# Kernel optimization log

Hardware: AMD Instinct MI355X
Metric: run time of the kernel (lower is better)

Reference implementation:

```python
import jax, jax.numpy as jnp
import numpy as np

N_NODES = 10000
N_EDGES = 640000
D = 128
N_GRAPHS = 16
N_CLASSES = 10


def setup_inputs() -> dict:
    key = jax.random.key(0)
    ks = jax.random.split(key, 12)
    x = jax.random.normal(ks[0], (N_NODES, D), dtype=jnp.float32)
    edge_index = jax.random.randint(ks[1], (2, N_EDGES), 0, N_NODES, dtype=jnp.int64)
    batch_ids = jnp.sort(jax.random.randint(ks[2], (N_NODES,), 0, N_GRAPHS, dtype=jnp.int64))
    s = 1.0 / np.sqrt(D)
    W_in = jax.random.normal(ks[3], (D, D), dtype=jnp.float32) * s
    W_self = jax.random.normal(ks[4], (D, D), dtype=jnp.float32) * s
    b = jnp.zeros((D,), dtype=jnp.float32)
    W_e1 = jax.random.normal(ks[5], (2 * D, D), dtype=jnp.float32) * (1.0 / np.sqrt(2 * D))
    b_e1 = jnp.zeros((D,), dtype=jnp.float32)
    W_e2 = jax.random.normal(ks[6], (D, 1), dtype=jnp.float32) * s
    b_e2 = jnp.zeros((1,), dtype=jnp.float32)
    W_cls = jax.random.normal(ks[7], (D, N_CLASSES), dtype=jnp.float32) * s
    b_cls = jnp.zeros((N_CLASSES,), dtype=jnp.float32)
    return {"x": x, "edge_index": edge_index, "batch_ids": batch_ids,
            "W_in": W_in, "W_self": W_self, "b": b,
            "W_e1": W_e1, "b_e1": b_e1, "W_e2": W_e2, "b_e2": b_e2,
            "W_cls": W_cls, "b_cls": b_cls}


def reference(x, edge_index, batch_ids, W_in, W_self, b, W_e1, b_e1, W_e2, b_e2, W_cls, b_cls):
    src, dst = edge_index[0], edge_index[1]
    # --- gnn(data) -> (z_node, z_graph) : GCN-style message passing ---
    h = x @ W_in                                  # [N, D]
    agg = jax.ops.segment_sum(h[src], dst, num_segments=N_NODES)  # [N, D]
    z_node = jax.nn.relu(agg + x @ W_self + b)    # [N, D]
    # mean pool per graph -> z_graph [B, D]
    sums = jax.ops.segment_sum(z_node, batch_ids, num_segments=N_GRAPHS)
    counts = jax.ops.segment_sum(jnp.ones((N_NODES,), dtype=z_node.dtype), batch_ids, num_segments=N_GRAPHS)
    z_graph = sums / jnp.maximum(counts, 1.0)[:, None]
    # --- edge predictor: gather, concat, MLP ---
    edge_features = jnp.concatenate([z_node[src], z_node[dst]], axis=1)  # [E, 2D]
    pred_edge = jax.nn.relu(edge_features @ W_e1 + b_e1) @ W_e2 + b_e2   # [E, 1]
    # --- classifier ---
    pred_class = z_graph @ W_cls + b_cls          # [B, n_classes]
    return (pred_edge, pred_class)
```

## Files before the change

kernel.cpp:

```cpp
#include <hip/hip_runtime.h>

#define N_NODES   10000
#define N_EDGES   640000
#define DIM       128
#define N_GRAPHS  16
#define N_CLASSES 10

typedef unsigned int uint;
typedef unsigned short ushort;

__device__ __forceinline__ float bf2f(uint lo16) {
    return __uint_as_float(lo16 << 16);
}
__device__ __forceinline__ ushort f2bf(float f) {
    uint u = __float_as_uint(f);
    u += 0x7fffu + ((u >> 16) & 1u);
    return (ushort)(u >> 16);
}

__global__ __launch_bounds__(256) void hist_dst(
    const int* __restrict__ dst, int* __restrict__ cnt)
{
    const int base = (blockIdx.x * 256 + threadIdx.x) * 4;
    const int d0 = dst[base + 0];
    const int d1 = dst[base + 1];
    const int d2 = dst[base + 2];
    const int d3 = dst[base + 3];
    atomicAdd(&cnt[d0], 1);
    atomicAdd(&cnt[d1], 1);
    atomicAdd(&cnt[d2], 1);
    atomicAdd(&cnt[d3], 1);
}

__global__ __launch_bounds__(256) void count_nodes(
    const int* __restrict__ bid, float* __restrict__ gcnt)
{
    __shared__ int h[N_GRAPHS];
    const int t = threadIdx.x;
    if (t < N_GRAPHS) h[t] = 0;
    __syncthreads();
    for (int n = t; n < N_NODES; n += 256) atomicAdd(&h[bid[n]], 1);
    __syncthreads();
    if (t < N_GRAPHS) gcnt[t] = (float)h[t];
}

__global__ __launch_bounds__(1024) void scan_k(
    const int* __restrict__ cnt, int* __restrict__ cursor)
{
    __shared__ int s[1024];
    const int t = threadIdx.x;
    int local[10];
    int sum = 0;
    if (t < 1000) {
        for (int j = 0; j < 10; ++j) { local[j] = sum; sum += cnt[t * 10 + j]; }
    }
    s[t] = (t < 1000) ? sum : 0;
    __syncthreads();
    for (int st = 1; st < 1024; st <<= 1) {
        int v = (t >= st) ? s[t - st] : 0;
        __syncthreads();
        s[t] += v;
        __syncthreads();
    }
    if (t < 1000) {
        const int off = (t == 0) ? 0 : s[t - 1];
        for (int j = 0; j < 10; ++j) cursor[t * 10 + j] = off + local[j];
    }
}

__global__ __launch_bounds__(256) void fill_csr(
    const int* __restrict__ src, const int* __restrict__ dst,
    int* __restrict__ cursor, uint* __restrict__ srcs)
{
    const int base = (blockIdx.x * 256 + threadIdx.x) * 4;
    const int d0 = dst[base + 0];
    const int d1 = dst[base + 1];
    const int d2 = dst[base + 2];
    const int d3 = dst[base + 3];
    const int s0 = src[base + 0];
    const int s1 = src[base + 1];
    const int s2 = src[base + 2];
    const int s3 = src[base + 3];
    const int p0 = atomicAdd(&cursor[d0], 1);
    const int p1 = atomicAdd(&cursor[d1], 1);
    const int p2 = atomicAdd(&cursor[d2], 1);
    const int p3 = atomicAdd(&cursor[d3], 1);
    srcs[p0] = (uint)s0;
    srcs[p1] = (uint)s1;
    srcs[p2] = (uint)s2;
    srcs[p3] = (uint)s3;
}

__global__ __launch_bounds__(256) void gather_x(
    const float* __restrict__ x,
    const int* __restrict__ cnt, const int* __restrict__ cursor,
    const uint* __restrict__ srcs,
    float* __restrict__ XAGG)
{
    const int n    = blockIdx.x * 4 + (threadIdx.x >> 6);
    const int lane = threadIdx.x & 63;
    const int end  = cursor[n];
    int i = end - cnt[n];

    float2 a0 = {0.f, 0.f}, a1 = {0.f, 0.f}, a2 = {0.f, 0.f}, a3 = {0.f, 0.f};
    const int co = lane * 2;

    for (; i + 4 <= end; i += 4) {
        const uint s0 = srcs[i], s1 = srcs[i + 1], s2 = srcs[i + 2], s3 = srcs[i + 3];
        const float2 r0 = *(const float2*)&x[s0 * DIM + co];
        const float2 r1 = *(const float2*)&x[s1 * DIM + co];
        const float2 r2 = *(const float2*)&x[s2 * DIM + co];
        const float2 r3 = *(const float2*)&x[s3 * DIM + co];
        a0.x += r0.x; a0.y += r0.y;
        a1.x += r1.x; a1.y += r1.y;
        a2.x += r2.x; a2.y += r2.y;
        a3.x += r3.x; a3.y += r3.y;
    }
    for (; i < end; ++i) {
        const float2 r = *(const float2*)&x[srcs[i] * DIM + co];
        a0.x += r.x; a0.y += r.y;
    }
    float2 s;
    s.x = (a0.x + a1.x) + (a2.x + a3.x);
    s.y = (a0.y + a1.y) + (a2.y + a3.y);
    *(float2*)&XAGG[n * DIM + co] = s;
}

__global__ __launch_bounds__(256) void gemm_z(
    const float* __restrict__ XAGG_in, const float* __restrict__ x,
    const float* __restrict__ W_in, const float* __restrict__ W_self,
    const float* __restrict__ b, const int* __restrict__ bid,
    float* __restrict__ Z, float* __restrict__ gsum)
{
    __shared__ float sa[16 * DIM];
    __shared__ float sb[16 * DIM];
    __shared__ int sbid[16];
    const int base = blockIdx.x * 16;
    const int t = threadIdx.x;
    {
        const float4* ga = (const float4*)(XAGG_in + base * DIM);
        const float4* gb = (const float4*)(x + base * DIM);
        float4* la = (float4*)sa;
        float4* lb = (float4*)sb;
        for (int i = t; i < 16 * DIM / 4; i += 256) { la[i] = ga[i]; lb[i] = gb[i]; }
        if (t < 16) sbid[t] = bid[base + t];
    }
    __syncthreads();

    const int half = t >> 7, c = t & 127;
    const float* __restrict__ W = half ? W_self : W_in;
    const float4* A4 = (const float4*)(half ? sb : sa);

    float acc[16];
#pragma unroll
    for (int r = 0; r < 16; ++r) acc[r] = 0.f;

    for (int k4 = 0; k4 < DIM / 4; ++k4) {
        const float w0 = W[(k4 * 4 + 0) * DIM + c];
        const float w1 = W[(k4 * 4 + 1) * DIM + c];
        const float w2 = W[(k4 * 4 + 2) * DIM + c];
        const float w3 = W[(k4 * 4 + 3) * DIM + c];
#pragma unroll
        for (int r = 0; r < 16; ++r) {
            const float4 xv = A4[r * (DIM / 4) + k4];
            acc[r] = fmaf(xv.x, w0, acc[r]);
            acc[r] = fmaf(xv.y, w1, acc[r]);
            acc[r] = fmaf(xv.z, w2, acc[r]);
            acc[r] = fmaf(xv.w, w3, acc[r]);
        }
    }
    __syncthreads();
    if (half) {
#pragma unroll
        for (int r = 0; r < 16; ++r) sa[r * DIM + c] = acc[r];
    }
    __syncthreads();
    if (!half) {
        const float bv = b[c];
        float run = 0.f;
        int cur = sbid[0];
#pragma unroll
        for (int r = 0; r < 16; ++r) {
            const float z = fmaxf(acc[r] + sa[r * DIM + c] + bv, 0.f);
            Z[(base + r) * DIM + c] = z;
            const int g = sbid[r];
            if (g != cur) { unsafeAtomicAdd(&gsum[cur * DIM + c], run); run = 0.f; cur = g; }
            run += z;
        }
        unsafeAtomicAdd(&gsum[cur * DIM + c], run);
    }
}

__global__ __launch_bounds__(256) void gemm_u12(
    const float* __restrict__ Z,
    const float* __restrict__ W_e1, const float* __restrict__ b_e1,
    ushort* __restrict__ U12)
{
    __shared__ float xs[16 * DIM];
    const int base = blockIdx.x * 16;
    const int t = threadIdx.x;
    {
        const float4* g = (const float4*)(Z + base * DIM);
        float4* l = (float4*)xs;
        for (int i = t; i < 16 * DIM / 4; i += 256) l[i] = g[i];
    }
    __syncthreads();

    const int half = t >> 7, c = t & 127;
    const float* __restrict__ W = W_e1 + half * 128 * DIM;
    const float4* A4 = (const float4*)xs;

    float acc[16];
#pragma unroll
    for (int r = 0; r < 16; ++r) acc[r] = 0.f;

    for (int k4 = 0; k4 < DIM / 4; ++k4) {
        const float w0 = W[(k4 * 4 + 0) * DIM + c];
        const float w1 = W[(k4 * 4 + 1) * DIM + c];
        const float w2 = W[(k4 * 4 + 2) * DIM + c];
        const float w3 = W[(k4 * 4 + 3) * DIM + c];
#pragma unroll
        for (int r = 0; r < 16; ++r) {
            const float4 xv = A4[r * (DIM / 4) + k4];
            acc[r] = fmaf(xv.x, w0, acc[r]);
            acc[r] = fmaf(xv.y, w1, acc[r]);
            acc[r] = fmaf(xv.z, w2, acc[r]);
            acc[r] = fmaf(xv.w, w3, acc[r]);
        }
    }
    const float bv = half ? 0.f : b_e1[c];
    for (int r = 0; r < 16; ++r)
        U12[(base + r) * 256 + half * 128 + c] = f2bf(acc[r] + bv);
}

__device__ __forceinline__ void ch2(uint a, uint b, float wl, float wh,
                                    float& accl, float& acch)
{
    const float fl = fmaxf(__uint_as_float(a << 16) + __uint_as_float(b << 16), 0.f);
    const float fh = fmaxf(__uint_as_float(a & 0xffff0000u) + __uint_as_float(b & 0xffff0000u), 0.f);
    accl = fmaf(fl, wl, accl);
    acch = fmaf(fh, wh, acch);
}

__global__ __launch_bounds__(256) void edge_mlp3(
    const ushort* __restrict__ U12,
    const int* __restrict__ src, const int* __restrict__ dst,
    const float* __restrict__ W_e2, const float* __restrict__ b_e2,
    float* __restrict__ out)
{
    __shared__ float ws[DIM];
    const int t = threadIdx.x;
    if (t < DIM) ws[t] = W_e2[t];
    __syncthreads();

    const int l16  = t & 15;
    const int grp  = t >> 4;
    const int e    = blockIdx.x * 16 + grp;

    const int s = src[e];
    const int d = dst[e];

    const uint4 a  = *(const uint4*)(U12 + s * 256 + l16 * 8);
    const uint4 bv = *(const uint4*)(U12 + d * 256 + 128 + l16 * 8);
    const float4 w0 = ((const float4*)ws)[l16 * 2 + 0];
    const float4 w1 = ((const float4*)ws)[l16 * 2 + 1];

    float acc0 = 0.f, acc1 = 0.f;
    ch2(a.x, bv.x, w0.x, w0.y, acc0, acc1);
    ch2(a.y, bv.y, w0.z, w0.w, acc0, acc1);
    ch2(a.z, bv.z, w1.x, w1.y, acc0, acc1);
    ch2(a.w, bv.w, w1.z, w1.w, acc0, acc1);

    float p = acc0 + acc1;
#pragma unroll
    for (int off = 8; off >= 1; off >>= 1)
        p += __shfl_xor(p, off);

    if (l16 == 0) out[e] = p + b_e2[0];
}

__global__ __launch_bounds__(256) void classify(
    const float* __restrict__ gsum, const float* __restrict__ gcnt,
    const float* __restrict__ W_cls, const float* __restrict__ b_cls,
    float* __restrict__ out)
{
    const int t = threadIdx.x;
    if (t >= N_GRAPHS * N_CLASSES) return;
    const int g = t / N_CLASSES;
    const int c = t % N_CLASSES;
    const float inv = 1.0f / fmaxf(gcnt[g], 1.0f);
    float acc = 0.f;
    for (int k = 0; k < DIM; ++k)
        acc += gsum[g * DIM + k] * W_cls[k * N_CLASSES + c];
    out[g * N_CLASSES + c] = acc * inv + b_cls[c];
}

extern "C" void kernel_launch(void* const* d_in, const int* in_sizes, int n_in,
                              void* d_out, int out_size, void* d_ws, size_t ws_size,
                              hipStream_t stream)
{
    const float* x      = (const float*)d_in[0];
    const int*   eidx   = (const int*)  d_in[1];
    const int*   bid    = (const int*)  d_in[2];
    const float* W_in   = (const float*)d_in[3];
    const float* W_self = (const float*)d_in[4];
    const float* b      = (const float*)d_in[5];
    const float* W_e1   = (const float*)d_in[6];
    const float* b_e1   = (const float*)d_in[7];
    const float* W_e2   = (const float*)d_in[8];
    const float* b_e2   = (const float*)d_in[9];
    const float* W_cls  = (const float*)d_in[10];
    const float* b_cls  = (const float*)d_in[11];
    float* out = (float*)d_out;

    char* ws = (char*)d_ws;
    int*    cnt    = (int*)   (ws);
    float*  gsum   = (float*) (ws + 40960);
    float*  gcnt   = (float*) (ws + 49152);
    int*    cursor = (int*)   (ws + 65536);
    uint*   srcs   = (uint*)  (ws + 131072);
    float*  XAGG   = (float*) (ws + 131072 + 2560000);
    ushort* U12    = (ushort*)(ws + 131072 + 7680000);

    const int* src = eidx;
    const int* dst = eidx + N_EDGES;

    hipMemsetAsync(d_ws, 0, 65536, stream);

    hist_dst   <<<N_EDGES / 1024, 256, 0, stream>>>(dst, cnt);
    count_nodes<<<1, 256, 0, stream>>>(bid, gcnt);
    scan_k     <<<1, 1024, 0, stream>>>(cnt, cursor);
    fill_csr   <<<N_EDGES / 1024, 256, 0, stream>>>(src, dst, cursor, srcs);
    gather_x   <<<N_NODES / 4, 256, 0, stream>>>(x, cnt, cursor, srcs, XAGG);
    gemm_z     <<<N_NODES / 16, 256, 0, stream>>>(XAGG, x, W_in, W_self, b, bid, XAGG, gsum);
    gemm_u12   <<<N_NODES / 16, 256, 0, stream>>>(XAGG, W_e1, b_e1, U12);
    edge_mlp3  <<<N_EDGES / 16, 256, 0, stream>>>(U12, src, dst, W_e2, b_e2, out);
    classify   <<<1, 256, 0, stream>>>(gsum, gcnt, W_cls, b_cls, out + N_EDGES);
}
```

Before: 293.4 us.

## Gather bf16 copy of x for aggregation and fuse node GEMMs into one kernel

Adds a pre-pass that converts x to bf16, and the neighbor-aggregation gather now reads these packed bf16 values, halving the bytes fetched per edge. It also fuses the z-node GEMM and the W_e1 projection into one kernel that keeps z in shared memory, so z is never written to or reread from global memory and one launch is dropped. The cost is an extra conversion kernel and reduced precision in the aggregated features, which may change numerics against the fp32 reference.

```diff
diff --git a/kernel.cpp b/kernel.cpp
--- a/kernel.cpp
+++ b/kernel.cpp
@@ -16,6 +16,16 @@
     uint u = __float_as_uint(f);
     u += 0x7fffu + ((u >> 16) & 1u);
     return (ushort)(u >> 16);
+}
+
+__global__ __launch_bounds__(256) void conv_bf16(
+    const float* __restrict__ x, uint* __restrict__ xb)
+{
+    const int idx = blockIdx.x * 256 + threadIdx.x;
+    const float4 v = ((const float4*)x)[idx];
+    uint lo = (uint)f2bf(v.x) | ((uint)f2bf(v.y) << 16);
+    uint hi = (uint)f2bf(v.z) | ((uint)f2bf(v.w) << 16);
+    ((uint2*)xb)[idx] = make_uint2(lo, hi);
 }
 
 __global__ __launch_bounds__(256) void hist_dst(
@@ -91,8 +101,8 @@
     srcs[p3] = (uint)s3;
 }
 
-__global__ __launch_bounds__(256) void gather_x(
-    const float* __restrict__ x,
+__global__ __launch_bounds__(256) void gather_xb(
+    const uint* __restrict__ xb,
     const int* __restrict__ cnt, const int* __restrict__ cursor,
     const uint* __restrict__ srcs,
     float* __restrict__ XAGG)
@@ -102,35 +112,36 @@
     const int end  = cursor[n];
     int i = end - cnt[n];
 
-    float2 a0 = {0.f, 0.f}, a1 = {0.f, 0.f}, a2 = {0.f, 0.f}, a3 = {0.f, 0.f};
-    const int co = lane * 2;
+    float a0 = 0.f, b0 = 0.f, a1 = 0.f, b1 = 0.f;
+    float a2 = 0.f, b2 = 0.f, a3 = 0.f, b3 = 0.f;
 
     for (; i + 4 <= end; i += 4) {
         const uint s0 = srcs[i], s1 = srcs[i + 1], s2 = srcs[i + 2], s3 = srcs[i + 3];
-        const float2 r0 = *(const float2*)&x[s0 * DIM + co];
-        const float2 r1 = *(const float2*)&x[s1 * DIM + co];
-        const float2 r2 = *(const float2*)&x[s2 * DIM + co];
-        const float2 r3 = *(const float2*)&x[s3 * DIM + co];
-        a0.x += r0.x; a0.y += r0.y;
-        a1.x += r1.x; a1.y += r1.y;
-        a2.x += r2.x; a2.y += r2.y;
-        a3.x += r3.x; a3.y += r3.y;
+        const uint v0 = xb[s0 * 64 + lane];
+        const uint v1 = xb[s1 * 64 + lane];
+        const uint v2 = xb[s2 * 64 + lane];
+        const uint v3 = xb[s3 * 64 + lane];
+        a0 += bf2f(v0 & 0xffffu); b0 += bf2f(v0 >> 16);
+        a1 += bf2f(v1 & 0xffffu); b1 += bf2f(v1 >> 16);
+        a2 += bf2f(v2 & 0xffffu); b2 += bf2f(v2 >> 16);
+        a3 += bf2f(v3 & 0xffffu); b3 += bf2f(v3 >> 16);
     }
     for (; i < end; ++i) {
-        const float2 r = *(const float2*)&x[srcs[i] * DIM + co];
-        a0.x += r.x; a0.y += r.y;
+        const uint v = xb[srcs[i] * 64 + lane];
+        a0 += bf2f(v & 0xffffu); b0 += bf2f(v >> 16);
     }
     float2 s;
-    s.x = (a0.x + a1.x) + (a2.x + a3.x);
-    s.y = (a0.y + a1.y) + (a2.y + a3.y);
-    *(float2*)&XAGG[n * DIM + co] = s;
-}
-
-__global__ __launch_bounds__(256) void gemm_z(
+    s.x = (a0 + a1) + (a2 + a3);
+    s.y = (b0 + b1) + (b2 + b3);
+    *(float2*)&XAGG[n * DIM + lane * 2] = s;
+}
+
+__global__ __launch_bounds__(256) void gemm_zu(
     const float* __restrict__ XAGG_in, const float* __restrict__ x,
     const float* __restrict__ W_in, const float* __restrict__ W_self,
     const float* __restrict__ b, const int* __restrict__ bid,
-    float* __restrict__ Z, float* __restrict__ gsum)
+    const float* __restrict__ W_e1, const float* __restrict__ b_e1,
+    float* __restrict__ gsum, ushort* __restrict__ U12)
 {
     __shared__ float sa[16 * DIM];
     __shared__ float sb[16 * DIM];
@@ -148,89 +159,74 @@
     __syncthreads();
 
     const int half = t >> 7, c = t & 127;
-    const float* __restrict__ W = half ? W_self : W_in;
-    const float4* A4 = (const float4*)(half ? sb : sa);
-
-    float acc[16];
-#pragma unroll
-    for (int r = 0; r < 16; ++r) acc[r] = 0.f;
-
-    for (int k4 = 0; k4 < DIM / 4; ++k4) {
-        const float w0 = W[(k4 * 4 + 0) * DIM + c];
-        const float w1 = W[(k4 * 4 + 1) * DIM + c];
-        const float w2 = W[(k4 * 4 + 2) * DIM + c];
-        const float w3 = W[(k4 * 4 + 3) * DIM + c];
-#pragma unroll
-        for (int r = 0; r < 16; ++r) {
-            const float4 xv = A4[r * (DIM / 4) + k4];
-            acc[r] = fmaf(xv.x, w0, acc[r]);
-            acc[r] = fmaf(xv.y, w1, acc[r]);
-            acc[r] = fmaf(xv.z, w2, acc[r]);
-            acc[r] = fmaf(xv.w, w3, acc[r]);
+
+    {
+        const float* __restrict__ W = half ? W_self : W_in;
+        const float4* A4 = (const float4*)(half ? sb : sa);
+        float acc[16];
+#pragma unroll
+        for (int r = 0; r < 16; ++r) acc[r] = 0.f;
+        for (int k4 = 0; k4 < DIM / 4; ++k4) {
+            const float w0 = W[(k4 * 4 + 0) * DIM + c];
+            const float w1 = W[(k4 * 4 + 1) * DIM + c];
+            const float w2 = W[(k4 * 4 + 2) * DIM + c];
+            const float w3 = W[(k4 * 4 + 3) * DIM + c];
+#pragma unroll
+            for (int r = 0; r < 16; ++r) {
+                const float4 xv = A4[r * (DIM / 4) + k4];
+                acc[r] = fmaf(xv.x, w0, acc[r]);
+                acc[r] = fmaf(xv.y, w1, acc[r]);
+                acc[r] = fmaf(xv.z, w2, acc[r]);
+                acc[r] = fmaf(xv.w, w3, acc[r]);
+            }
         }
-    }
-    __syncthreads();
-    if (half) {
-#pragma unroll
-        for (int r = 0; r < 16; ++r) sa[r * DIM + c] = acc[r];
-    }
-    __syncthreads();
-    if (!half) {
-        const float bv = b[c];
-        float run = 0.f;
-        int cur = sbid[0];
-#pragma unroll
-        for (int r = 0; r < 16; ++r) {
-            const float z = fmaxf(acc[r] + sa[r * DIM + c] + bv, 0.f);
-            Z[(base + r) * DIM + c] = z;
-            const int g = sbid[r];
-            if (g != cur) { unsafeAtomicAdd(&gsum[cur * DIM + c], run); run = 0.f; cur = g; }
-            run += z;
+        __syncthreads();
+        if (half) {
+#pragma unroll
+            for (int r = 0; r < 16; ++r) sb[r * DIM + c] = acc[r];
         }
-        unsafeAtomicAdd(&gsum[cur * DIM + c], run);
-    }
-}
-
-__global__ __launch_bounds__(256) void gemm_u12(
-    const float* __restrict__ Z,
-    const float* __restrict__ W_e1, const float* __restrict__ b_e1,
-    ushort* __restrict__ U12)
-{
-    __shared__ float xs[16 * DIM];
-    const int base = blockIdx.x * 16;
-    const int t = threadIdx.x;
+        __syncthreads();
+        if (!half) {
+            const float bv = b[c];
+            float run = 0.f;
+            int cur = sbid[0];
+#pragma unroll
+            for (int r = 0; r < 16; ++r) {
+                const float z = fmaxf(acc[r] + sb[r * DIM + c] + bv, 0.f);
+                sa[r * DIM + c] = z;
+                const int g = sbid[r];
+                if (g != cur) { unsafeAtomicAdd(&gsum[cur * DIM + c], run); run = 0.f; cur = g; }
+                run += z;
+            }
+            unsafeAtomicAdd(&gsum[cur * DIM + c], run);
+        }
+        __syncthreads();
+    }
+
     {
-        const float4* g = (const float4*)(Z + base * DIM);
-        float4* l = (float4*)xs;
-        for (int i = t; i < 16 * DIM / 4; i += 256) l[i] = g[i];
-    }
-    __syncthreads();
-
-    const int half = t >> 7, c = t & 127;
-    const float* __restrict__ W = W_e1 + half * 128 * DIM;
-    const float4* A4 = (const float4*)xs;
-
-    float acc[16];
-#pragma unroll
-    for (int r = 0; r < 16; ++r) acc[r] = 0.f;
-
-    for (int k4 = 0; k4 < DIM / 4; ++k4) {
-        const float w0 = W[(k4 * 4 + 0) * DIM + c];
-        const float w1 = W[(k4 * 4 + 1) * DIM + c];
-        const float w2 = W[(k4 * 4 + 2) * DIM + c];
-        const float w3 = W[(k4 * 4 + 3) * DIM + c];
-#pragma unroll
-        for (int r = 0; r < 16; ++r) {
-            const float4 xv = A4[r * (DIM / 4) + k4];
-            acc[r] = fmaf(xv.x, w0, acc[r]);
-            acc[r] = fmaf(xv.y, w1, acc[r]);
-            acc[r] = fmaf(xv.z, w2, acc[r]);
-            acc[r] = fmaf(xv.w, w3, acc[r]);
+        const float* __restrict__ W = W_e1 + half * 128 * DIM;
+        const float4* Z4 = (const float4*)sa;
+        float acc[16];
+#pragma unroll
+        for (int r = 0; r < 16; ++r) acc[r] = 0.f;
+        for (int k4 = 0; k4 < DIM / 4; ++k4) {
+            const float w0 = W[(k4 * 4 + 0) * DIM + c];
+            const float w1 = W[(k4 * 4 + 1) * DIM + c];
+            const float w2 = W[(k4 * 4 + 2) * DIM + c];
+            const float w3 = W[(k4 * 4 + 3) * DIM + c];
+#pragma unroll
+            for (int r = 0; r < 16; ++r) {
+                const float4 xv = Z4[r * (DIM / 4) + k4];
+                acc[r] = fmaf(xv.x, w0, acc[r]);
+                acc[r] = fmaf(xv.y, w1, acc[r]);
+                acc[r] = fmaf(xv.z, w2, acc[r]);
+                acc[r] = fmaf(xv.w, w3, acc[r]);
+            }
         }
-    }
-    const float bv = half ? 0.f : b_e1[c];
-    for (int r = 0; r < 16; ++r)
-        U12[(base + r) * 256 + half * 128 + c] = f2bf(acc[r] + bv);
+        const float bv = half ? 0.f : b_e1[c];
+        for (int r = 0; r < 16; ++r)
+            U12[(base + r) * 256 + half * 128 + c] = f2bf(acc[r] + bv);
+    }
 }
 
 __device__ __forceinline__ void ch2(uint a, uint b, float wl, float wh,
@@ -321,19 +317,21 @@
     uint*   srcs   = (uint*)  (ws + 131072);
     float*  XAGG   = (float*) (ws + 131072 + 2560000);
     ushort* U12    = (ushort*)(ws + 131072 + 7680000);
+    uint*   xb     = (uint*)  (ws + 131072 + 12800000);
 
     const int* src = eidx;
     const int* dst = eidx + N_EDGES;
 
     hipMemsetAsync(d_ws, 0, 65536, stream);
 
+    conv_bf16  <<<(N_NODES * DIM / 4) / 256, 256, 0, stream>>>(x, xb);
     hist_dst   <<<N_EDGES / 1024, 256, 0, stream>>>(dst, cnt);
     count_nodes<<<1, 256, 0, stream>>>(bid, gcnt);
     scan_k     <<<1, 1024, 0, stream>>>(cnt, cursor);
     fill_csr   <<<N_EDGES / 1024, 256, 0, stream>>>(src, dst, cursor, srcs);
-    gather_x   <<<N_NODES / 4, 256, 0, stream>>>(x, cnt, cursor, srcs, XAGG);
-    gemm_z     <<<N_NODES / 16, 256, 0, stream>>>(XAGG, x, W_in, W_self, b, bid, XAGG, gsum);
-    gemm_u12   <<<N_NODES / 16, 256, 0, stream>>>(XAGG, W_e1, b_e1, U12);
+    gather_xb  <<<N_NODES / 4, 256, 0, stream>>>(xb, cnt, cursor, srcs, XAGG);
+    gemm_zu    <<<N_NODES / 16, 256, 0, stream>>>(XAGG, x, W_in, W_self, b, bid,
+                                                  W_e1, b_e1, gsum, U12);
     edge_mlp3  <<<N_EDGES / 16, 256, 0, stream>>>(U12, src, dst, W_e2, b_e2, out);
     classify   <<<1, 256, 0, stream>>>(gsum, gcnt, W_cls, b_cls, out + N_EDGES);
 }
```

After: 280.9 us. -4.3%, faster.
